# Performance work log

Measured on AMD Instinct MI355X. Metric: run time of the kernel, lower is better.

The kernel has to match this reference:

```python
import jax, jax.numpy as jnp
import numpy as np

D_MODEL, N_HEADS, D_FF = 768, 12, 3072
B, T = 4, 2048
EPS = 1e-5


def setup_inputs() -> dict:
    key = jax.random.key(0)
    ks = jax.random.split(key, 12)
    s = 0.02
    inp = {
        'x': jax.random.normal(ks[0], (B, T, D_MODEL), jnp.float32),
        'mask': jnp.tril(jnp.ones((1, 1, T, T), jnp.bool_)),  # causal decoder mask
        'ln1_g': jnp.ones((D_MODEL,), jnp.float32),
        'ln1_b': jnp.zeros((D_MODEL,), jnp.float32),
        'Wq': jax.random.normal(ks[1], (D_MODEL, D_MODEL), jnp.float32) * s,
        'bq': jnp.zeros((D_MODEL,), jnp.float32),
        'Wk': jax.random.normal(ks[2], (D_MODEL, D_MODEL), jnp.float32) * s,
        'bk': jnp.zeros((D_MODEL,), jnp.float32),
        'Wv': jax.random.normal(ks[3], (D_MODEL, D_MODEL), jnp.float32) * s,
        'bv': jnp.zeros((D_MODEL,), jnp.float32),
        'Wo': jax.random.normal(ks[4], (D_MODEL, D_MODEL), jnp.float32) * s,
        'bo': jnp.zeros((D_MODEL,), jnp.float32),
        'ln2_g': jnp.ones((D_MODEL,), jnp.float32),
        'ln2_b': jnp.zeros((D_MODEL,), jnp.float32),
        'W1': jax.random.normal(ks[5], (D_MODEL, D_FF), jnp.float32) * s,
        'b1': jnp.zeros((D_FF,), jnp.float32),
        'W2': jax.random.normal(ks[6], (D_FF, D_MODEL), jnp.float32) * s,
        'b2': jnp.zeros((D_MODEL,), jnp.float32),
    }
    return inp


def _layer_norm(x, g, b):
    mu = jnp.mean(x, axis=-1, keepdims=True)
    var = jnp.mean(jnp.square(x - mu), axis=-1, keepdims=True)
    return (x - mu) * jax.lax.rsqrt(var + EPS) * g + b


def reference(x, mask, ln1_g, ln1_b, Wq, bq, Wk, bk, Wv, bv, Wo, bo,
              ln2_g, ln2_b, W1, b1, W2, b2):
    Bx, Tx, _ = x.shape
    d_k = D_MODEL // N_HEADS
    # --- attention sublayer (pre-norm) ---
    h = _layer_norm(x, ln1_g, ln1_b)
    q = (h @ Wq + bq).reshape(Bx, Tx, N_HEADS, d_k).transpose(0, 2, 1, 3)
    k = (h @ Wk + bk).reshape(Bx, Tx, N_HEADS, d_k).transpose(0, 2, 1, 3)
    v = (h @ Wv + bv).reshape(Bx, Tx, N_HEADS, d_k).transpose(0, 2, 1, 3)
    scores = jnp.einsum('bhqd,bhkd->bhqk', q, k) / jnp.sqrt(jnp.float32(d_k))
    scores = jnp.where(mask, scores, -jnp.inf)
    weights = jax.nn.softmax(scores, axis=-1)
    attn = jnp.einsum('bhqk,bhkd->bhqd', weights, v)
    attn = attn.transpose(0, 2, 1, 3).reshape(Bx, Tx, D_MODEL)
    x = x + (attn @ Wo + bo)
    # --- FFN sublayer (pre-norm) ---
    h = _layer_norm(x, ln2_g, ln2_b)
    h = jax.nn.gelu(h @ W1 + b1, approximate=False)
    return x + (h @ W2 + b2)
```

## Files before the change

### kernel.cpp

```cpp
#include <hip/hip_runtime.h>

#define DEV __device__ __forceinline__

typedef __attribute__((ext_vector_type(8))) short short8;
typedef __attribute__((ext_vector_type(4))) float f32x4;
typedef __attribute__((ext_vector_type(4))) unsigned int u32x4;
typedef __attribute__((ext_vector_type(2))) unsigned int u32x2;
typedef __attribute__((ext_vector_type(4))) unsigned short u16x4;

constexpr int Bc = 4, Tc = 2048, Dm = 768, Hh = 12, DK = 64, DFF = 3072;
constexpr int MT = Bc * Tc;

DEV unsigned short f2bf(float f) {
  unsigned int u = __float_as_uint(f);
  u += 0x7fff + ((u >> 16) & 1);
  return (unsigned short)(u >> 16);
}

DEV unsigned cvt_pk_bf16(float lo, float hi) {
  unsigned r;
  asm("v_cvt_pk_bf16_f32 %0, %1, %2" : "=v"(r) : "v"(lo), "v"(hi));
  return r;
}

DEV void gload_lds16(const void* g, void* l) {
  __builtin_amdgcn_global_load_lds(
      (const __attribute__((address_space(1))) void*)g,
      (__attribute__((address_space(3))) void*)l, 16, 0, 0);
}

__global__ __launch_bounds__(256) void ln_kernel(const float* __restrict__ x,
    const float* __restrict__ gam, const float* __restrict__ bet,
    unsigned short* __restrict__ out)
{
  int lane = threadIdx.x & 63;
  int row = blockIdx.x * 4 + (threadIdx.x >> 6);
  const float* xr = x + (size_t)row * Dm + lane * 12;
  f32x4 v0 = *(const f32x4*)(xr);
  f32x4 v1 = *(const f32x4*)(xr + 4);
  f32x4 v2 = *(const f32x4*)(xr + 8);
  float s = 0.f, s2 = 0.f;
#pragma unroll
  for (int j = 0; j < 4; j++) {
    s  += v0[j] + v1[j] + v2[j];
    s2 += v0[j]*v0[j] + v1[j]*v1[j] + v2[j]*v2[j];
  }
#pragma unroll
  for (int off = 32; off; off >>= 1) { s += __shfl_xor(s, off); s2 += __shfl_xor(s2, off); }
  float mu = s * (1.f / Dm);
  float inv = rsqrtf(s2 * (1.f / Dm) - mu * mu + 1e-5f);
  int cb = lane * 12;
  unsigned short o[12];
#pragma unroll
  for (int j = 0; j < 4; j++) {
    o[j]     = f2bf((v0[j] - mu) * inv * gam[cb + j]     + bet[cb + j]);
    o[4 + j] = f2bf((v1[j] - mu) * inv * gam[cb + 4 + j] + bet[cb + 4 + j]);
    o[8 + j] = f2bf((v2[j] - mu) * inv * gam[cb + 8 + j] + bet[cb + 8 + j]);
  }
  unsigned short* orow = out + (size_t)row * Dm + cb;
#pragma unroll
  for (int i = 0; i < 3; i++) *(u16x4*)(orow + i * 4) = *(const u16x4*)(&o[i * 4]);
}

__global__ __launch_bounds__(256) void wtrans_all_kernel(
    const float* __restrict__ Wq, const float* __restrict__ Wk,
    const float* __restrict__ Wv, const float* __restrict__ Wo,
    const float* __restrict__ W1, const float* __restrict__ W2,
    unsigned short* wq_t, unsigned short* wk_t, unsigned short* wv_t,
    unsigned short* wo_t, unsigned short* w1_t, unsigned short* w2_t)
{
  __shared__ unsigned short tile[32][33];
  int bid = blockIdx.x;
  const float* src; unsigned short* dst; int K, N, t;
  if (bid < 2304) {
    int w = bid / 576; t = bid % 576; K = Dm; N = Dm;
    src = w == 0 ? Wq : w == 1 ? Wk : w == 2 ? Wv : Wo;
    dst = w == 0 ? wq_t : w == 1 ? wk_t : w == 2 ? wv_t : wo_t;
  } else if (bid < 4608) {
    t = bid - 2304; K = Dm; N = DFF; src = W1; dst = w1_t;
  } else {
    t = bid - 4608; K = DFF; N = Dm; src = W2; dst = w2_t;
  }
  int gx = N / 32;
  int n0 = (t % gx) * 32, k0 = (t / gx) * 32;
  int tx = threadIdx.x & 31, ty = threadIdx.x >> 5;
#pragma unroll
  for (int i = 0; i < 4; i++) {
    int kr = ty * 4 + i;
    tile[kr][tx] = f2bf(src[(size_t)(k0 + kr) * N + n0 + tx]);
  }
  __syncthreads();
#pragma unroll
  for (int i = 0; i < 4; i++) {
    int nr = ty * 4 + i;
    dst[(size_t)(n0 + nr) * K + k0 + tx] = tile[tx][nr];
  }
}

template<int OUT_MODE>
DEV void gemm_body(unsigned short* As, unsigned short* Bs,
    const unsigned short* __restrict__ A, const unsigned short* __restrict__ Bt,
    const float* __restrict__ bias, const float* __restrict__ resid, void* __restrict__ out,
    int M, int N, int K)
{
  int m0 = blockIdx.x * 128, n0 = blockIdx.y * 128;
  int tid = threadIdx.x, lane = tid & 63, wid = tid >> 6;
  int wr = wid >> 1, wc = wid & 1;
  int fr = lane & 15, fg = lane >> 4;
  f32x4 acc[4][4] = {};
  for (int k0 = 0; k0 < K; k0 += 64) {
    __syncthreads();
#pragma unroll
    for (int p = 0; p < 4; p++) {
      int L = wid * 256 + p * 64 + lane;
      int row = L >> 3, pos = L & 7;
      int ch = pos ^ (row & 7);
      gload_lds16(&A[(size_t)(m0 + row) * K + k0 + ch * 8],
                  &As[(size_t)(wid * 256 + p * 64) * 8]);
      gload_lds16(&Bt[(size_t)(n0 + row) * K + k0 + ch * 8],
                  &Bs[(size_t)(wid * 256 + p * 64) * 8]);
    }
    __syncthreads();
#pragma unroll
    for (int kk = 0; kk < 2; kk++) {
      short8 af[4], bfr[4];
#pragma unroll
      for (int m = 0; m < 4; m++) {
        int row = wr * 64 + m * 16 + fr;
        int ch = (kk * 4 + fg) ^ (fr & 7);
        af[m] = *(const short8*)(&As[row * 64 + ch * 8]);
      }
#pragma unroll
      for (int n = 0; n < 4; n++) {
        int row = wc * 64 + n * 16 + fr;
        int ch = (kk * 4 + fg) ^ (fr & 7);
        bfr[n] = *(const short8*)(&Bs[row * 64 + ch * 8]);
      }
#pragma unroll
      for (int m = 0; m < 4; m++)
#pragma unroll
        for (int n = 0; n < 4; n++)
          acc[m][n] = __builtin_amdgcn_mfma_f32_16x16x32_bf16(af[m], bfr[n], acc[m][n], 0, 0, 0);
    }
  }
  int col = fr, rbase = fg * 4;
#pragma unroll
  for (int m = 0; m < 4; m++) {
#pragma unroll
    for (int n = 0; n < 4; n++) {
      int gn = n0 + wc * 64 + n * 16 + col;
      float bv = bias[gn];
      if (OUT_MODE == 4) {
        int gm0 = m0 + wr * 64 + m * 16 + rbase;
        int b = gm0 >> 11, t = gm0 & 2047, h = gn >> 6, d = gn & 63;
        u16x4 pk;
#pragma unroll
        for (int rr = 0; rr < 4; rr++) pk[rr] = f2bf(acc[m][n][rr] + bv);
        *(u16x4*)(&((unsigned short*)out)[(((size_t)b * Hh + h) * DK + d) * Tc + t]) = pk;
      } else {
#pragma unroll
        for (int rr = 0; rr < 4; rr++) {
          int gm = m0 + wr * 64 + m * 16 + rbase + rr;
          float v = acc[m][n][rr] + bv;
          if (OUT_MODE == 2) v = 0.5f * v * (1.f + erff(v * 0.70710678118f));
          if (OUT_MODE == 0) {
            v += resid[(size_t)gm * N + gn];
            ((float*)out)[(size_t)gm * N + gn] = v;
          } else if (OUT_MODE == 3) {
            int b = gm >> 11, t = gm & 2047, h = gn >> 6, d = gn & 63;
            ((unsigned short*)out)[(((size_t)b * Hh + h) * Tc + t) * DK + d] = f2bf(v);
          } else {
            ((unsigned short*)out)[(size_t)gm * N + gn] = f2bf(v);
          }
        }
      }
    }
  }
}

__global__ __launch_bounds__(256) void gemm_f32out_kernel(const unsigned short* A,
    const unsigned short* Bt, const float* bias, const float* resid, float* out,
    int M, int N, int K)
{
  __shared__ unsigned short As[128 * 64], Bs[128 * 64];
  gemm_body<0>(As, Bs, A, Bt, bias, resid, out, M, N, K);
}

__global__ __launch_bounds__(256) void gemm_gelu_kernel(const unsigned short* A,
    const unsigned short* Bt, const float* bias, unsigned short* out,
    int M, int N, int K)
{
  __shared__ unsigned short As[128 * 64], Bs[128 * 64];
  gemm_body<2>(As, Bs, A, Bt, bias, nullptr, out, M, N, K);
}

__global__ __launch_bounds__(256) void gemm_qkv_kernel(const unsigned short* A,
    const unsigned short* Bq, const unsigned short* Bk, const unsigned short* Bv,
    const float* bq, const float* bk, const float* bv,
    unsigned short* oq, unsigned short* okh, unsigned short* ovt)
{
  __shared__ unsigned short As[128 * 64], Bs[128 * 64];
  if (blockIdx.z == 0)      gemm_body<1>(As, Bs, A, Bq, bq, nullptr, oq,  MT, Dm, Dm);
  else if (blockIdx.z == 1) gemm_body<3>(As, Bs, A, Bk, bk, nullptr, okh, MT, Dm, Dm);
  else                      gemm_body<4>(As, Bs, A, Bv, bv, nullptr, ovt, MT, Dm, Dm);
}

__global__ __launch_bounds__(256) void attn_kernel(const unsigned short* __restrict__ q,
    const unsigned short* __restrict__ kh, const unsigned short* __restrict__ vt,
    unsigned short* __restrict__ o)
{
  __shared__ unsigned short Ks[2][64 * 64], Vs[2][64 * 64];
  __shared__ unsigned short P_lds[4][16 * 64];
  int lane = threadIdx.x & 63, wid = threadIdx.x >> 6;
  int fr = lane & 15, fg = lane >> 4;
  int bid = blockIdx.x;
  int xcd = bid & 7, ii = bid >> 3;
  int bh = xcd * 6 + (ii >> 5);
  int qc = 31 - (ii & 31);
  int b = bh / Hh, h = bh - b * Hh;
  int q0 = qc * 64 + wid * 16;
  const size_t qbase = ((size_t)b * Tc) * Dm + h * DK;
  const unsigned short* kg = kh + (size_t)bh * Tc * DK;
  const unsigned short* vg = vt + (size_t)bh * DK * Tc;
  short8 qa0 = *(const short8*)(&q[qbase + (size_t)(q0 + fr) * Dm + fg * 8]);
  short8 qa1 = *(const short8*)(&q[qbase + (size_t)(q0 + fr) * Dm + 32 + fg * 8]);
  f32x4 oa[4] = {};
  f32x4 rs = {};
  short8 onesb;
#pragma unroll
  for (int j = 0; j < 8; j++) onesb[j] = (short)0x3F80;
  unsigned short* Pw = P_lds[wid];
  int nIter = qc + 1;

#define STAGE(buf, kk0)                                                          \
  {                                                                              \
    _Pragma("unroll")                                                            \
    for (int c = 0; c < 2; c++) {                                                \
      int L = c * 256 + wid * 64 + lane;                                         \
      int row = L >> 3, cc = (L & 7) ^ (row & 7);                                \
      gload_lds16(kg + (size_t)((kk0) + row) * DK + cc * 8,                      \
                  &Ks[buf][(size_t)(c * 256 + wid * 64) * 8]);                   \
      gload_lds16(vg + (size_t)row * Tc + (kk0) + cc * 8,                        \
                  &Vs[buf][(size_t)(c * 256 + wid * 64) * 8]);                   \
    }                                                                            \
  }

  STAGE(0, 0)
  for (int it = 0; it < nIter; it++) {
    int cur = it & 1;
    if (it + 1 < nIter) {
      STAGE(cur ^ 1, (it + 1) * 64)
      asm volatile("s_waitcnt vmcnt(4)" ::: "memory");
    } else {
      asm volatile("s_waitcnt vmcnt(0)" ::: "memory");
    }
    __builtin_amdgcn_s_barrier();
    int k0 = it * 64;
    f32x4 st[4];
#pragma unroll
    for (int t = 0; t < 4; t++) {
      int row = t * 16 + fr;
      short8 kf0 = *(const short8*)(&Ks[cur][row * 64 + ((fg)     ^ (fr & 7)) * 8]);
      short8 kf1 = *(const short8*)(&Ks[cur][row * 64 + ((4 + fg) ^ (fr & 7)) * 8]);
      st[t] = {};
      st[t] = __builtin_amdgcn_mfma_f32_16x16x32_bf16(kf0, qa0, st[t], 0, 0, 0);
      st[t] = __builtin_amdgcn_mfma_f32_16x16x32_bf16(kf1, qa1, st[t], 0, 0, 0);
    }
    short8 vb[4][2];
#pragma unroll
    for (int dg = 0; dg < 4; dg++) {
      int row = dg * 16 + fr;
#pragma unroll
      for (int hf = 0; hf < 2; hf++)
        vb[dg][hf] = *(const short8*)(&Vs[cur][row * 64 + ((hf * 4 + fg) ^ (fr & 7)) * 8]);
    }
    bool masked = (it == nIter - 1);
#pragma unroll
    for (int t = 0; t < 4; t++) {
      float p[4];
#pragma unroll
      for (int rr = 0; rr < 4; rr++) {
        float e = __expf(st[t][rr] * 0.125f);
        if (masked) {
          int key = k0 + t * 16 + fg * 4 + rr;
          e = (key <= q0 + fr) ? e : 0.f;
        }
        p[rr] = e;
      }
      u32x2 pkw;
      pkw[0] = cvt_pk_bf16(p[0], p[1]);
      pkw[1] = cvt_pk_bf16(p[2], p[3]);
      int C = t * 2 + (fg >> 1);
      *(u32x2*)(&Pw[fr * 64 + ((C ^ (fr & 7)) << 3) + ((fg & 1) << 2)]) = pkw;
    }
    asm volatile("s_waitcnt lgkmcnt(0)" ::: "memory");
    __builtin_amdgcn_sched_barrier(0);
    short8 pa0 = *(const short8*)(&Pw[fr * 64 + ((fg     ^ (fr & 7)) * 8)]);
    short8 pa1 = *(const short8*)(&Pw[fr * 64 + (((4 + fg) ^ (fr & 7)) * 8)]);
    rs = __builtin_amdgcn_mfma_f32_16x16x32_bf16(pa0, onesb, rs, 0, 0, 0);
    rs = __builtin_amdgcn_mfma_f32_16x16x32_bf16(pa1, onesb, rs, 0, 0, 0);
#pragma unroll
    for (int dg = 0; dg < 4; dg++) {
      oa[dg] = __builtin_amdgcn_mfma_f32_16x16x32_bf16(pa0, vb[dg][0], oa[dg], 0, 0, 0);
      oa[dg] = __builtin_amdgcn_mfma_f32_16x16x32_bf16(pa1, vb[dg][1], oa[dg], 0, 0, 0);
    }
    __builtin_amdgcn_s_barrier();
  }
#undef STAGE
#pragma unroll
  for (int dg = 0; dg < 4; dg++)
#pragma unroll
    for (int rr = 0; rr < 4; rr++) {
      int qi = q0 + fg * 4 + rr;
      o[qbase + (size_t)qi * Dm + dg * 16 + fr] = f2bf(oa[dg][rr] / rs[rr]);
    }
}

extern "C" void kernel_launch(void* const* d_in, const int* in_sizes, int n_in,
                              void* d_out, int out_size, void* d_ws, size_t ws_size,
                              hipStream_t stream) {
  const float* x     = (const float*)d_in[0];
  const float* ln1_g = (const float*)d_in[2];
  const float* ln1_b = (const float*)d_in[3];
  const float* Wq = (const float*)d_in[4];  const float* bq = (const float*)d_in[5];
  const float* Wk = (const float*)d_in[6];  const float* bk = (const float*)d_in[7];
  const float* Wv = (const float*)d_in[8];  const float* bv = (const float*)d_in[9];
  const float* Wo = (const float*)d_in[10]; const float* bo = (const float*)d_in[11];
  const float* ln2_g = (const float*)d_in[12];
  const float* ln2_b = (const float*)d_in[13];
  const float* W1 = (const float*)d_in[14]; const float* b1 = (const float*)d_in[15];
  const float* W2 = (const float*)d_in[16]; const float* b2 = (const float*)d_in[17];
  float* out = (float*)d_out;

  char* ws = (char*)d_ws;
  const size_t HB = (size_t)MT * Dm * 2;
  unsigned short* h_buf  = (unsigned short*)(ws);
  unsigned short* q_buf  = (unsigned short*)(ws + HB);
  unsigned short* kh_buf = (unsigned short*)(ws + 2 * HB);
  unsigned short* vt_buf = (unsigned short*)(ws + 3 * HB);
  unsigned short* wq_t   = (unsigned short*)(ws + 4 * HB);
  unsigned short* wk_t   = wq_t + (size_t)Dm * Dm;
  unsigned short* wv_t   = wk_t + (size_t)Dm * Dm;
  unsigned short* wo_t   = wv_t + (size_t)Dm * Dm;
  unsigned short* w1_t   = wo_t + (size_t)Dm * Dm;
  unsigned short* w2_t   = w1_t + (size_t)Dm * DFF;
  unsigned short* g_buf  = w2_t + (size_t)DFF * Dm;

  wtrans_all_kernel<<<dim3(6912), 256, 0, stream>>>(
      Wq, Wk, Wv, Wo, W1, W2, wq_t, wk_t, wv_t, wo_t, w1_t, w2_t);

  ln_kernel<<<MT / 4, 256, 0, stream>>>(x, ln1_g, ln1_b, h_buf);
  gemm_qkv_kernel<<<dim3(MT / 128, Dm / 128, 3), 256, 0, stream>>>(
      h_buf, wq_t, wk_t, wv_t, bq, bk, bv, q_buf, kh_buf, vt_buf);
  attn_kernel<<<dim3(1536), 256, 0, stream>>>(q_buf, kh_buf, vt_buf, h_buf);
  gemm_f32out_kernel<<<dim3(MT / 128, Dm / 128), 256, 0, stream>>>(
      h_buf, wo_t, bo, x, out, MT, Dm, Dm);
  ln_kernel<<<MT / 4, 256, 0, stream>>>(out, ln2_g, ln2_b, h_buf);
  gemm_gelu_kernel<<<dim3(MT / 128, DFF / 128), 256, 0, stream>>>(
      h_buf, w1_t, b1, g_buf, MT, DFF, Dm);
  gemm_f32out_kernel<<<dim3(MT / 128, Dm / 128), 256, 0, stream>>>(
      g_buf, w2_t, b2, out, out, MT, Dm, DFF);
}
```

Baseline: 272.5 us.

## Add 256x256-tile 8-wave pipelined GEMM for QKV and FFN-up projections

Adds a new GEMM body with 256x256 output tiles, 512 threads and 128KB of dynamic LDS. It double-buffers the K-slabs with direct global-to-LDS loads, interleaved with four quadrant MFMA clusters gated by barriers and s_setprio. The QKV and GELU GEMMs switch to this kernel to raise data reuse per tile and overlap loads with compute. The tradeoff is fewer blocks: the QKV launch has 288 blocks and the GELU launch 384. The heavy LDS use may also limit occupancy and leave tail effects.

```diff
diff --git a/kernel.cpp b/kernel.cpp
--- a/kernel.cpp
+++ b/kernel.cpp
@@ -150,23 +150,163 @@
     for (int n = 0; n < 4; n++) {
       int gn = n0 + wc * 64 + n * 16 + col;
       float bv = bias[gn];
+#pragma unroll
+      for (int rr = 0; rr < 4; rr++) {
+        int gm = m0 + wr * 64 + m * 16 + rbase + rr;
+        float v = acc[m][n][rr] + bv;
+        if (OUT_MODE == 2) v = 0.5f * v * (1.f + erff(v * 0.70710678118f));
+        if (OUT_MODE == 0) {
+          v += resid[(size_t)gm * N + gn];
+          ((float*)out)[(size_t)gm * N + gn] = v;
+        } else {
+          ((unsigned short*)out)[(size_t)gm * N + gn] = f2bf(v);
+        }
+      }
+    }
+  }
+}
+
+__global__ __launch_bounds__(256) void gemm_f32out_kernel(const unsigned short* A,
+    const unsigned short* Bt, const float* bias, const float* resid, float* out,
+    int M, int N, int K)
+{
+  __shared__ unsigned short As[128 * 64], Bs[128 * 64];
+  gemm_body<0>(As, Bs, A, Bt, bias, resid, out, M, N, K);
+}
+
+
+DEV void stage_half(const unsigned short* src, int ldK, unsigned short* ldsbase, int tid) {
+#pragma unroll
+  for (int c = 0; c < 2; c++) {
+    int q = c * 512 + tid;
+    int row = q >> 3, pos = q & 7;
+    int ch = pos ^ (row & 7);
+    gload_lds16(src + (size_t)row * ldK + ch * 8, ldsbase + q * 8);
+  }
+}
+
+template<int QM>
+DEV void loadA_frags(short8 af[4][2], const unsigned short* Ac, int wr, int fr, int fg) {
+#pragma unroll
+  for (int m = 0; m < 4; m++)
+#pragma unroll
+    for (int kk = 0; kk < 2; kk++) {
+      int R = QM * 128 + wr * 64 + m * 16 + fr;
+      af[m][kk] = *(const short8*)(Ac + R * 64 + (((kk * 4 + fg) ^ (R & 7)) << 3));
+    }
+}
+
+template<int QN>
+DEV void loadB_frags(short8 bf[2][2], const unsigned short* Bcc, int wc, int fr, int fg) {
+#pragma unroll
+  for (int n = 0; n < 2; n++)
+#pragma unroll
+    for (int kk = 0; kk < 2; kk++) {
+      int S = QN * 128 + wc * 32 + n * 16 + fr;
+      bf[n][kk] = *(const short8*)(Bcc + S * 64 + (((kk * 4 + fg) ^ (S & 7)) << 3));
+    }
+}
+
+DEV void phase_begin() {
+  __builtin_amdgcn_s_barrier();
+  asm volatile("s_waitcnt lgkmcnt(0)" ::: "memory");
+  __builtin_amdgcn_sched_barrier(0);
+  __builtin_amdgcn_s_setprio(1);
+}
+DEV void phase_end() {
+  __builtin_amdgcn_s_setprio(0);
+  __builtin_amdgcn_s_barrier();
+}
+
+template<int QM, int QN>
+DEV void mfma_cluster(f32x4 acc[8][4], const short8 af[4][2], const short8 bf[2][2]) {
+#pragma unroll
+  for (int m = 0; m < 4; m++)
+#pragma unroll
+    for (int n = 0; n < 2; n++)
+#pragma unroll
+      for (int kk = 0; kk < 2; kk++)
+        acc[QM * 4 + m][QN * 2 + n] = __builtin_amdgcn_mfma_f32_16x16x32_bf16(
+            af[m][kk], bf[n][kk], acc[QM * 4 + m][QN * 2 + n], 0, 0, 0);
+}
+
+template<int OUT_MODE>
+DEV void gemm256_body(unsigned short* lds,
+    const unsigned short* __restrict__ A, const unsigned short* __restrict__ Bt,
+    const float* __restrict__ bias, void* __restrict__ out, int N, int K)
+{
+  int tid = threadIdx.x, lane = tid & 63, wid = tid >> 6;
+  int wr = wid >> 2, wc = wid & 3;
+  int fr = lane & 15, fg = lane >> 4;
+  int bm = blockIdx.x * 256, bn = blockIdx.y * 256;
+  const int nT = K >> 6;
+  f32x4 acc[8][4] = {};
+  short8 af[4][2], bf[2][2];
+
+  stage_half(A  + (size_t)bm * K,         K, lds + 0,             tid);
+  stage_half(Bt + (size_t)bn * K,         K, lds + 16384,         tid);
+  stage_half(Bt + (size_t)(bn + 128) * K, K, lds + 16384 + 8192,  tid);
+  stage_half(A  + (size_t)(bm + 128) * K, K, lds + 8192,          tid);
+  asm volatile("s_waitcnt vmcnt(4)" ::: "memory");
+  __builtin_amdgcn_s_barrier();
+
+  for (int t = 0; t < nT; t++) {
+    int c = t & 1;
+    unsigned short* Ac = lds + c * 32768;
+    unsigned short* Bcc = Ac + 16384;
+    unsigned short* An = lds + (c ^ 1) * 32768;
+    unsigned short* Bn = An + 16384;
+    const unsigned short* Asrc = A  + (size_t)bm * K + (t + 1) * 64;
+    const unsigned short* Bsrc = Bt + (size_t)bn * K + (t + 1) * 64;
+    bool more = (t + 1 < nT);
+    loadA_frags<0>(af, Ac, wr, fr, fg);
+    loadB_frags<0>(bf, Bcc, wc, fr, fg);
+    if (more) {
+      stage_half(Asrc, K, An, tid);
+      asm volatile("s_waitcnt vmcnt(4)" ::: "memory");
+    } else {
+      asm volatile("s_waitcnt vmcnt(2)" ::: "memory");
+    }
+    phase_begin(); mfma_cluster<0, 0>(acc, af, bf); phase_end();
+    loadB_frags<1>(bf, Bcc, wc, fr, fg);
+    if (more) {
+      stage_half(Bsrc, K, Bn, tid);
+      asm volatile("s_waitcnt vmcnt(4)" ::: "memory");
+    } else {
+      asm volatile("s_waitcnt vmcnt(0)" ::: "memory");
+    }
+    phase_begin(); mfma_cluster<0, 1>(acc, af, bf); phase_end();
+    loadA_frags<1>(af, Ac, wr, fr, fg);
+    if (more) stage_half(Bsrc + (size_t)128 * K, K, Bn + 8192, tid);
+    phase_begin(); mfma_cluster<1, 1>(acc, af, bf); phase_end();
+    loadB_frags<0>(bf, Bcc, wc, fr, fg);
+    if (more) {
+      stage_half(Asrc + (size_t)128 * K, K, An + 8192, tid);
+      asm volatile("s_waitcnt vmcnt(4)" ::: "memory");
+    }
+    phase_begin(); mfma_cluster<1, 0>(acc, af, bf); phase_end();
+  }
+
+#pragma unroll
+  for (int i = 0; i < 8; i++) {
+#pragma unroll
+    for (int j = 0; j < 4; j++) {
+      int gm0 = bm + (i >> 2) * 128 + wr * 64 + (i & 3) * 16 + fg * 4;
+      int gn  = bn + (j >> 1) * 128 + wc * 32 + (j & 1) * 16 + fr;
+      float bv = bias[gn];
       if (OUT_MODE == 4) {
-        int gm0 = m0 + wr * 64 + m * 16 + rbase;
         int b = gm0 >> 11, t = gm0 & 2047, h = gn >> 6, d = gn & 63;
         u16x4 pk;
 #pragma unroll
-        for (int rr = 0; rr < 4; rr++) pk[rr] = f2bf(acc[m][n][rr] + bv);
+        for (int rr = 0; rr < 4; rr++) pk[rr] = f2bf(acc[i][j][rr] + bv);
         *(u16x4*)(&((unsigned short*)out)[(((size_t)b * Hh + h) * DK + d) * Tc + t]) = pk;
       } else {
 #pragma unroll
         for (int rr = 0; rr < 4; rr++) {
-          int gm = m0 + wr * 64 + m * 16 + rbase + rr;
-          float v = acc[m][n][rr] + bv;
+          int gm = gm0 + rr;
+          float v = acc[i][j][rr] + bv;
           if (OUT_MODE == 2) v = 0.5f * v * (1.f + erff(v * 0.70710678118f));
-          if (OUT_MODE == 0) {
-            v += resid[(size_t)gm * N + gn];
-            ((float*)out)[(size_t)gm * N + gn] = v;
-          } else if (OUT_MODE == 3) {
+          if (OUT_MODE == 3) {
             int b = gm >> 11, t = gm & 2047, h = gn >> 6, d = gn & 63;
             ((unsigned short*)out)[(((size_t)b * Hh + h) * Tc + t) * DK + d] = f2bf(v);
           } else {
@@ -178,31 +318,23 @@
   }
 }
 
-__global__ __launch_bounds__(256) void gemm_f32out_kernel(const unsigned short* A,
-    const unsigned short* Bt, const float* bias, const float* resid, float* out,
-    int M, int N, int K)
-{
-  __shared__ unsigned short As[128 * 64], Bs[128 * 64];
-  gemm_body<0>(As, Bs, A, Bt, bias, resid, out, M, N, K);
-}
-
-__global__ __launch_bounds__(256) void gemm_gelu_kernel(const unsigned short* A,
-    const unsigned short* Bt, const float* bias, unsigned short* out,
-    int M, int N, int K)
-{
-  __shared__ unsigned short As[128 * 64], Bs[128 * 64];
-  gemm_body<2>(As, Bs, A, Bt, bias, nullptr, out, M, N, K);
-}
-
-__global__ __launch_bounds__(256) void gemm_qkv_kernel(const unsigned short* A,
-    const unsigned short* Bq, const unsigned short* Bk, const unsigned short* Bv,
-    const float* bq, const float* bk, const float* bv,
+__global__ __launch_bounds__(512, 2) void gemm256_qkv_kernel(
+    const unsigned short* A, const unsigned short* Bq, const unsigned short* Bk,
+    const unsigned short* Bv, const float* bq, const float* bk, const float* bv,
     unsigned short* oq, unsigned short* okh, unsigned short* ovt)
 {
-  __shared__ unsigned short As[128 * 64], Bs[128 * 64];
-  if (blockIdx.z == 0)      gemm_body<1>(As, Bs, A, Bq, bq, nullptr, oq,  MT, Dm, Dm);
-  else if (blockIdx.z == 1) gemm_body<3>(As, Bs, A, Bk, bk, nullptr, okh, MT, Dm, Dm);
-  else                      gemm_body<4>(As, Bs, A, Bv, bv, nullptr, ovt, MT, Dm, Dm);
+  extern __shared__ unsigned short lds[];
+  if (blockIdx.z == 0)      gemm256_body<1>(lds, A, Bq, bq, oq,  Dm, Dm);
+  else if (blockIdx.z == 1) gemm256_body<3>(lds, A, Bk, bk, okh, Dm, Dm);
+  else                      gemm256_body<4>(lds, A, Bv, bv, ovt, Dm, Dm);
+}
+
+__global__ __launch_bounds__(512, 2) void gemm256_gelu_kernel(
+    const unsigned short* A, const unsigned short* Bt, const float* bias,
+    unsigned short* out)
+{
+  extern __shared__ unsigned short lds[];
+  gemm256_body<2>(lds, A, Bt, bias, out, DFF, Dm);
 }
 
 __global__ __launch_bounds__(256) void attn_kernel(const unsigned short* __restrict__ q,
@@ -346,18 +478,27 @@
   unsigned short* w2_t   = w1_t + (size_t)Dm * DFF;
   unsigned short* g_buf  = w2_t + (size_t)DFF * Dm;
 
+  static bool attr_set = []() {
+    hipFuncSetAttribute((const void*)gemm256_qkv_kernel,
+                        hipFuncAttributeMaxDynamicSharedMemorySize, 131072);
+    hipFuncSetAttribute((const void*)gemm256_gelu_kernel,
+                        hipFuncAttributeMaxDynamicSharedMemorySize, 131072);
+    return true;
+  }();
+  (void)attr_set;
+
   wtrans_all_kernel<<<dim3(6912), 256, 0, stream>>>(
       Wq, Wk, Wv, Wo, W1, W2, wq_t, wk_t, wv_t, wo_t, w1_t, w2_t);
 
   ln_kernel<<<MT / 4, 256, 0, stream>>>(x, ln1_g, ln1_b, h_buf);
-  gemm_qkv_kernel<<<dim3(MT / 128, Dm / 128, 3), 256, 0, stream>>>(
+  gemm256_qkv_kernel<<<dim3(MT / 256, Dm / 256, 3), 512, 131072, stream>>>(
       h_buf, wq_t, wk_t, wv_t, bq, bk, bv, q_buf, kh_buf, vt_buf);
   attn_kernel<<<dim3(1536), 256, 0, stream>>>(q_buf, kh_buf, vt_buf, h_buf);
   gemm_f32out_kernel<<<dim3(MT / 128, Dm / 128), 256, 0, stream>>>(
       h_buf, wo_t, bo, x, out, MT, Dm, Dm);
   ln_kernel<<<MT / 4, 256, 0, stream>>>(out, ln2_g, ln2_b, h_buf);
-  gemm_gelu_kernel<<<dim3(MT / 128, DFF / 128), 256, 0, stream>>>(
-      h_buf, w1_t, b1, g_buf, MT, DFF, Dm);
+  gemm256_gelu_kernel<<<dim3(MT / 256, DFF / 256), 512, 131072, stream>>>(
+      h_buf, w1_t, b1, g_buf);
   gemm_f32out_kernel<<<dim3(MT / 128, Dm / 128), 256, 0, stream>>>(
       g_buf, w2_t, b2, out, out, MT, Dm, DFF);
 }
```

After: 287.4 us. +5.5%, slower.
